# Kernel optimization log

Measured on AMD Instinct MI355X. Metric: run time of the kernel, lower is better.

The kernel has to match this reference:

```python
import jax, jax.numpy as jnp
import numpy as np
import math

N_HEADS = 16
EMBED = 1024
D_HEAD = EMBED // N_HEADS
B, L = 2, 2048


def setup_inputs() -> dict:
    key = jax.random.key(0)
    k1, k2, k3, k4, k5 = jax.random.split(key, 5)
    s = 0.02
    return {
        "x": jax.random.normal(k1, (B, L, EMBED), dtype=jnp.float32),
        "w_qkv": jax.random.normal(k2, (3 * EMBED, EMBED), dtype=jnp.float32) * s,
        "b_qkv": jax.random.normal(k3, (3 * EMBED,), dtype=jnp.float32) * s,
        "w_out": jax.random.normal(k4, (EMBED, EMBED), dtype=jnp.float32) * s,
        "b_out": jax.random.normal(k5, (EMBED,), dtype=jnp.float32) * s,
        "mask": 1,
    }


def reference(x, w_qkv, b_qkv, w_out, b_out, mask):
    b, l, e = x.shape
    qkv = x @ w_qkv.T + b_qkv                      # (B, L, 3E)
    q, k, v = jnp.split(qkv, 3, axis=-1)
    # (B, L, H, d) -> (B, H, L, d)
    q = q.reshape(b, l, N_HEADS, D_HEAD).transpose(0, 2, 1, 3)
    k = k.reshape(b, l, N_HEADS, D_HEAD).transpose(0, 2, 1, 3)
    v = v.reshape(b, l, N_HEADS, D_HEAD).transpose(0, 2, 1, 3)
    # NOTE: faithful to source bug -- scores use V, not K
    scores = jnp.einsum("bhld,bhmd->bhlm", q, v) * (1.0 / math.sqrt(D_HEAD))
    if mask:
        causal = jnp.triu(jnp.ones((l, l), dtype=bool), k=1)  # (L, L)
        scores = jnp.where(causal, -jnp.inf, scores)
    attn = jax.nn.softmax(scores, axis=-1)          # (B, H, L, L)
    out = jnp.einsum("bhlm,bhmd->bhld", attn, v)    # (B, H, L, d)
    # NOTE: faithful to source bug -- transpose(1,2) result discarded,
    # so reshape straight from (B, H, L, d) to (B, L, E)
    out = out.reshape(b, l, e)
    return out @ w_out.T + b_out
```

## Files before the change

kernel.cpp:

```cpp
#include <hip/hip_runtime.h>
#include <math.h>

constexpr int Lc = 2048, Ec = 1024, Hc = 16, Dc = 64;

typedef __attribute__((ext_vector_type(8))) short bf16x8;
typedef __attribute__((ext_vector_type(4))) float f32x4;
typedef unsigned short u16;
typedef unsigned int u32;

#define MFMA16(a, b, c) __builtin_amdgcn_mfma_f32_16x16x32_bf16(a, b, c, 0, 0, 0)

__device__ inline u16 f2bf(float f) {
  u32 u = __builtin_bit_cast(u32, f);
  u32 r = u + 0x7fff + ((u >> 16) & 1);
  return (u16)(r >> 16);
}

__device__ inline void gld16(const void* g, void* l) {
  __builtin_amdgcn_global_load_lds(
      (const __attribute__((address_space(1))) u32*)g,
      (__attribute__((address_space(3))) u32*)l, 16, 0, 0);
}

constexpr size_t XN = (size_t)4096 * 1024;
constexpr size_t WQN = (size_t)2048 * 1024;
constexpr size_t WON = (size_t)1024 * 1024;

__global__ __launch_bounds__(256) void convert_all(
    const float* __restrict__ x, const float* __restrict__ wqkv,
    const float* __restrict__ wout, u16* __restrict__ xb,
    u16* __restrict__ wqb, u16* __restrict__ wob)
{
  const size_t i = ((size_t)blockIdx.x * 256 + threadIdx.x) * 4;
  float4 v;
  u16* dst;
  if (i < XN) {
    v = *(const float4*)(x + i);
    dst = xb + i;
  } else if (i < XN + WQN) {
    const size_t off = i - XN;
    const size_t row = off >> 10, col = off & 1023;
    const size_t srow = row + ((row >> 10) << 10);
    v = *(const float4*)(wqkv + srow * 1024 + col);
    dst = wqb + off;
  } else {
    const size_t off = i - XN - WQN;
    v = *(const float4*)(wout + off);
    dst = wob + off;
  }
  u16 o0 = f2bf(v.x), o1 = f2bf(v.y), o2 = f2bf(v.z), o3 = f2bf(v.w);
  dst[0] = o0; dst[1] = o1; dst[2] = o2; dst[3] = o3;
}

__global__ __launch_bounds__(256) void gemm_qv(
    const u16* __restrict__ A, const u16* __restrict__ W,
    const float* __restrict__ bqkv, u16* __restrict__ Q, u16* __restrict__ V)
{
  __shared__ u16 As[128 * 32];
  __shared__ u16 Bs[128 * 32];
  const int tid = threadIdx.x;
  const int w = tid >> 6, lane = tid & 63;
  const int quad = lane >> 4, l16 = lane & 15;
  const int wm = w >> 1, wn = w & 1;
  const int rowTile = blockIdx.y * 128;
  const int colTile = blockIdx.x * 128;

  const int r0 = tid >> 2, o0 = (tid & 3) * 8;
  const u16* Ab0 = A + (size_t)(rowTile + r0) * 1024 + o0;
  const u16* Ab1 = A + (size_t)(rowTile + r0 + 64) * 1024 + o0;
  const u16* Bb0 = W + (size_t)(colTile + r0) * 1024 + o0;
  const u16* Bb1 = W + (size_t)(colTile + r0 + 64) * 1024 + o0;
  u16* lA0 = &As[(size_t)tid * 8];
  u16* lA1 = &As[(size_t)(tid + 256) * 8];
  u16* lB0 = &Bs[(size_t)tid * 8];
  u16* lB1 = &Bs[(size_t)(tid + 256) * 8];

  f32x4 acc[4][4] = {};

  for (int k0 = 0; k0 < 1024; k0 += 32) {
    __syncthreads();
    gld16(Ab0 + k0, lA0);
    gld16(Ab1 + k0, lA1);
    gld16(Bb0 + k0, lB0);
    gld16(Bb1 + k0, lB1);
    __syncthreads();
    bf16x8 af[4], bf[4];
#pragma unroll
    for (int s = 0; s < 4; ++s)
      af[s] = *(const bf16x8*)&As[(wm * 64 + s * 16 + l16) * 32 + quad * 8];
#pragma unroll
    for (int n = 0; n < 4; ++n)
      bf[n] = *(const bf16x8*)&Bs[(wn * 64 + n * 16 + l16) * 32 + quad * 8];
#pragma unroll
    for (int s = 0; s < 4; ++s)
#pragma unroll
      for (int n = 0; n < 4; ++n)
        acc[s][n] = MFMA16(af[s], bf[n], acc[s][n]);
  }

#pragma unroll
  for (int n = 0; n < 4; ++n) {
    const int gn = colTile + wn * 64 + n * 16 + l16;
    const bool isV = gn >= 1024;
    const float bias = bqkv[gn + (isV ? 1024 : 0)];
    const float scl = isV ? 1.0f : 0.125f;
    const int h = (gn & 1023) >> 6, d = gn & 63;
    u16* dst = isV ? V : Q;
#pragma unroll
    for (int s = 0; s < 4; ++s) {
#pragma unroll
      for (int r = 0; r < 4; ++r) {
        const int gm = rowTile + wm * 64 + s * 16 + quad * 4 + r;
        const int b = gm >> 11, l = gm & 2047;
        dst[(((size_t)(b * Hc + h)) * Lc + l) * Dc + d] = f2bf((acc[s][n][r] + bias) * scl);
      }
    }
  }
}

constexpr int VSTR = 72;
constexpr int VTSTR = 66;
constexpr int PSTR = 72;

__global__ __launch_bounds__(256) void attn_mfma(
    const u16* __restrict__ Q, const u16* __restrict__ V,
    u16* __restrict__ outA)
{
  __shared__ u16 Vs[64 * VSTR];
  __shared__ u16 VsT[64 * VTSTR];
  __shared__ u16 Ps[4][16 * PSTR];
  const int tid = threadIdx.x;
  const int w = tid >> 6, lane = tid & 63;
  const int quad = lane >> 4, l16 = lane & 15;
  const int bh = blockIdx.y;
  const int b = bh >> 4, h = bh & 15;
  const u16* Qb = Q + (size_t)bh * Lc * Dc;
  const u16* Vb = V + (size_t)bh * Lc * Dc;
  const int vr0 = tid >> 3, vd0 = (tid & 7) * 8;

  for (int half = 0; half < 2; ++half) {
    const int qt = half ? (31 - blockIdx.x) : blockIdx.x;
    const int q0 = qt * 64;
    const int nt = qt + 1;
    const int wqmin = q0 + w * 16;

    bf16x8 qf[2];
#pragma unroll
    for (int kk = 0; kk < 2; ++kk)
      qf[kk] = *(const bf16x8*)(Qb + (size_t)(q0 + w * 16 + l16) * 64 + kk * 32 + quad * 8);

    f32x4 O[4] = {};
    float lsum[4] = {0.f, 0.f, 0.f, 0.f};

    bf16x8 v0 = *(const bf16x8*)(Vb + (size_t)vr0 * 64 + vd0);
    bf16x8 v1 = *(const bf16x8*)(Vb + (size_t)(vr0 + 32) * 64 + vd0);

    for (int t = 0; t < nt; ++t) {
      const int kt = t * 64;
      __syncthreads();
      *(bf16x8*)&Vs[vr0 * VSTR + vd0] = v0;
      *(bf16x8*)&Vs[(vr0 + 32) * VSTR + vd0] = v1;
#pragma unroll
      for (int j = 0; j < 8; ++j) {
        VsT[(vd0 + j) * VTSTR + vr0] = (u16)v0[j];
        VsT[(vd0 + j) * VTSTR + vr0 + 32] = (u16)v1[j];
      }
      if (t + 1 < nt) {
        v0 = *(const bf16x8*)(Vb + (size_t)(kt + 64 + vr0) * 64 + vd0);
        v1 = *(const bf16x8*)(Vb + (size_t)(kt + 96 + vr0) * 64 + vd0);
      }
      __syncthreads();
      if (kt > wqmin + 15) continue;

      f32x4 sf[4] = {};
      bf16x8 bvf[2][4];
#pragma unroll
      for (int nb = 0; nb < 4; ++nb)
#pragma unroll
        for (int kk = 0; kk < 2; ++kk)
          bvf[kk][nb] = *(const bf16x8*)&Vs[(nb * 16 + l16) * VSTR + kk * 32 + quad * 8];
#pragma unroll
      for (int nb = 0; nb < 4; ++nb) {
        sf[nb] = MFMA16(qf[0], bvf[0][nb], sf[nb]);
        sf[nb] = MFMA16(qf[1], bvf[1][nb], sf[nb]);
      }

      const bool needmask = (kt + 63 > wqmin);
#pragma unroll
      for (int nb = 0; nb < 4; ++nb)
#pragma unroll
        for (int r = 0; r < 4; ++r) {
          float p = __expf(sf[nb][r]);
          if (needmask) {
            const int key = kt + nb * 16 + l16;
            const int qr = wqmin + quad * 4 + r;
            if (key > qr) p = 0.f;
          }
          lsum[r] += p;
          Ps[w][(quad * 4 + r) * PSTR + nb * 16 + l16] = f2bf(p);
        }

      bf16x8 pf[2];
#pragma unroll
      for (int kk = 0; kk < 2; ++kk)
        pf[kk] = *(const bf16x8*)&Ps[w][l16 * PSTR + kk * 32 + quad * 8];
#pragma unroll
      for (int db = 0; db < 4; ++db) {
        O[db] = MFMA16(pf[0], *(const bf16x8*)&VsT[(db * 16 + l16) * VTSTR + quad * 8], O[db]);
        O[db] = MFMA16(pf[1], *(const bf16x8*)&VsT[(db * 16 + l16) * VTSTR + 32 + quad * 8], O[db]);
      }
    }

#pragma unroll
    for (int r = 0; r < 4; ++r) {
      float l = lsum[r];
      l += __shfl_xor(l, 1);
      l += __shfl_xor(l, 2);
      l += __shfl_xor(l, 4);
      l += __shfl_xor(l, 8);
      const float inv = 1.f / l;
      const int q = q0 + w * 16 + quad * 4 + r;
      const int orow = h * 128 + (q >> 4);
      const int cbase = (q & 15) << 6;
#pragma unroll
      for (int db = 0; db < 4; ++db)
        outA[((size_t)b * Lc + orow) * Ec + cbase + db * 16 + l16] =
            f2bf(O[db][r] * inv);
    }
  }
}

__global__ __launch_bounds__(256) void gemm_out(
    const u16* __restrict__ A, const u16* __restrict__ W,
    const float* __restrict__ bias, float* __restrict__ out)
{
  __shared__ u16 As[128 * 32];
  __shared__ u16 Bs[128 * 32];
  const int tid = threadIdx.x;
  const int w = tid >> 6, lane = tid & 63;
  const int quad = lane >> 4, l16 = lane & 15;
  const int wm = w >> 1, wn = w & 1;
  const int rowTile = blockIdx.y * 128;
  const int colTile = blockIdx.x * 128;

  const int r0 = tid >> 2, o0 = (tid & 3) * 8;
  const u16* Ab0 = A + (size_t)(rowTile + r0) * 1024 + o0;
  const u16* Ab1 = A + (size_t)(rowTile + r0 + 64) * 1024 + o0;
  const u16* Bb0 = W + (size_t)(colTile + r0) * 1024 + o0;
  const u16* Bb1 = W + (size_t)(colTile + r0 + 64) * 1024 + o0;
  u16* lA0 = &As[(size_t)tid * 8];
  u16* lA1 = &As[(size_t)(tid + 256) * 8];
  u16* lB0 = &Bs[(size_t)tid * 8];
  u16* lB1 = &Bs[(size_t)(tid + 256) * 8];

  f32x4 acc[4][4] = {};

  for (int k0 = 0; k0 < 1024; k0 += 32) {
    __syncthreads();
    gld16(Ab0 + k0, lA0);
    gld16(Ab1 + k0, lA1);
    gld16(Bb0 + k0, lB0);
    gld16(Bb1 + k0, lB1);
    __syncthreads();
    bf16x8 af[4], bf[4];
#pragma unroll
    for (int s = 0; s < 4; ++s)
      af[s] = *(const bf16x8*)&As[(wm * 64 + s * 16 + l16) * 32 + quad * 8];
#pragma unroll
    for (int n = 0; n < 4; ++n)
      bf[n] = *(const bf16x8*)&Bs[(wn * 64 + n * 16 + l16) * 32 + quad * 8];
#pragma unroll
    for (int s = 0; s < 4; ++s)
#pragma unroll
      for (int n = 0; n < 4; ++n)
        acc[s][n] = MFMA16(af[s], bf[n], acc[s][n]);
  }

#pragma unroll
  for (int n = 0; n < 4; ++n) {
    const int gn = colTile + wn * 64 + n * 16 + l16;
    const float bn = bias[gn];
#pragma unroll
    for (int s = 0; s < 4; ++s)
#pragma unroll
      for (int r = 0; r < 4; ++r) {
        const int gm = rowTile + wm * 64 + s * 16 + quad * 4 + r;
        out[(size_t)gm * 1024 + gn] = acc[s][n][r] + bn;
      }
  }
}

extern "C" void kernel_launch(void* const* d_in, const int* in_sizes, int n_in,
                              void* d_out, int out_size, void* d_ws, size_t ws_size,
                              hipStream_t stream) {
  (void)in_sizes; (void)n_in; (void)out_size; (void)ws_size;
  const float* x     = (const float*)d_in[0];
  const float* w_qkv = (const float*)d_in[1];
  const float* b_qkv = (const float*)d_in[2];
  const float* w_out = (const float*)d_in[3];
  const float* b_out = (const float*)d_in[4];
  float* out = (float*)d_out;

  u16* xb  = (u16*)d_ws;
  u16* wqb = xb + XN;
  u16* wob = wqb + WQN;
  u16* Qw  = wob + WON;
  u16* Vw  = Qw + (size_t)2 * Hc * Lc * Dc;
  u16* Aw  = Vw + (size_t)2 * Hc * Lc * Dc;

  convert_all<<<7168, 256, 0, stream>>>(x, w_qkv, w_out, xb, wqb, wob);
  gemm_qv<<<dim3(16, 32), 256, 0, stream>>>(xb, wqb, b_qkv, Qw, Vw);
  attn_mfma<<<dim3(16, 32), 256, 0, stream>>>(Qw, Vw, Aw);
  gemm_out<<<dim3(8, 32), 256, 0, stream>>>(Aw, wob, b_out, out);
}
```

Baseline: 193.4 us.

## Restructure attention to 256-query blocks with transposed MFMA and smaller out-GEMM tiles

The attention kernel now gives each block 256 queries and each wave 64 rows. It computes S^T with V fragments taken straight from global memory, stages only a swizzled transposed V tile in LDS, and writes P with packed stores. This drops the untransposed V staging and the two-half load-balancing loop, and reuses each V tile across four query subtiles. It also removes the LDS bank conflicts on VsT. Because blocks now cover causal ranges of very different length, the load may be less balanced. The output GEMM tile shrinks to 64x128 so more blocks are launched.

```diff
diff --git a/kernel.cpp b/kernel.cpp
--- a/kernel.cpp
+++ b/kernel.cpp
@@ -118,114 +118,130 @@
   }
 }
 
-constexpr int VSTR = 72;
-constexpr int VTSTR = 66;
-constexpr int PSTR = 72;
-
-__global__ __launch_bounds__(256) void attn_mfma(
+constexpr int VTSTR = 72;
+constexpr int PSTR = 88;
+
+__global__ __launch_bounds__(256, 1) void attn_mfma(
     const u16* __restrict__ Q, const u16* __restrict__ V,
     u16* __restrict__ outA)
 {
-  __shared__ u16 Vs[64 * VSTR];
   __shared__ u16 VsT[64 * VTSTR];
-  __shared__ u16 Ps[4][16 * PSTR];
+  __shared__ u16 Ps[256 * PSTR];
   const int tid = threadIdx.x;
   const int w = tid >> 6, lane = tid & 63;
   const int quad = lane >> 4, l16 = lane & 15;
+  const int q0 = blockIdx.x * 256;
   const int bh = blockIdx.y;
   const int b = bh >> 4, h = bh & 15;
   const u16* Qb = Q + (size_t)bh * Lc * Dc;
   const u16* Vb = V + (size_t)bh * Lc * Dc;
+  const int wq0 = q0 + w * 64;
+  const int nt = (q0 >> 6) + 4;
+
+  bf16x8 qf[4][2];
+#pragma unroll
+  for (int s = 0; s < 4; ++s)
+#pragma unroll
+    for (int kk = 0; kk < 2; ++kk)
+      qf[s][kk] = *(const bf16x8*)(Qb + (size_t)(wq0 + s * 16 + l16) * 64 + kk * 32 + quad * 8);
+
+  f32x4 O[4][4] = {};
+  float lsum[4] = {0.f, 0.f, 0.f, 0.f};
+
   const int vr0 = tid >> 3, vd0 = (tid & 7) * 8;
-
-  for (int half = 0; half < 2; ++half) {
-    const int qt = half ? (31 - blockIdx.x) : blockIdx.x;
-    const int q0 = qt * 64;
-    const int nt = qt + 1;
-    const int wqmin = q0 + w * 16;
-
-    bf16x8 qf[2];
+  bf16x8 v0 = *(const bf16x8*)(Vb + (size_t)vr0 * 64 + vd0);
+  bf16x8 v1 = *(const bf16x8*)(Vb + (size_t)(vr0 + 32) * 64 + vd0);
+  bf16x8 av[4][2];
+#pragma unroll
+  for (int nb = 0; nb < 4; ++nb)
 #pragma unroll
     for (int kk = 0; kk < 2; ++kk)
-      qf[kk] = *(const bf16x8*)(Qb + (size_t)(q0 + w * 16 + l16) * 64 + kk * 32 + quad * 8);
-
-    f32x4 O[4] = {};
-    float lsum[4] = {0.f, 0.f, 0.f, 0.f};
-
-    bf16x8 v0 = *(const bf16x8*)(Vb + (size_t)vr0 * 64 + vd0);
-    bf16x8 v1 = *(const bf16x8*)(Vb + (size_t)(vr0 + 32) * 64 + vd0);
-
-    for (int t = 0; t < nt; ++t) {
-      const int kt = t * 64;
-      __syncthreads();
-      *(bf16x8*)&Vs[vr0 * VSTR + vd0] = v0;
-      *(bf16x8*)&Vs[(vr0 + 32) * VSTR + vd0] = v1;
-#pragma unroll
-      for (int j = 0; j < 8; ++j) {
-        VsT[(vd0 + j) * VTSTR + vr0] = (u16)v0[j];
-        VsT[(vd0 + j) * VTSTR + vr0 + 32] = (u16)v1[j];
-      }
-      if (t + 1 < nt) {
-        v0 = *(const bf16x8*)(Vb + (size_t)(kt + 64 + vr0) * 64 + vd0);
-        v1 = *(const bf16x8*)(Vb + (size_t)(kt + 96 + vr0) * 64 + vd0);
-      }
-      __syncthreads();
-      if (kt > wqmin + 15) continue;
-
+      av[nb][kk] = *(const bf16x8*)(Vb + (size_t)(nb * 16 + l16) * 64 + kk * 32 + quad * 8);
+
+  for (int t = 0; t < nt; ++t) {
+    const int kt = t * 64;
+    __syncthreads();
+#pragma unroll
+    for (int j = 0; j < 8; ++j) {
+      const int d = vd0 + j, sw = d & 0x38;
+      VsT[d * VTSTR + (vr0 ^ sw)] = (u16)v0[j];
+      VsT[d * VTSTR + ((vr0 + 32) ^ sw)] = (u16)v1[j];
+    }
+    if (t + 1 < nt) {
+      v0 = *(const bf16x8*)(Vb + (size_t)(kt + 64 + vr0) * 64 + vd0);
+      v1 = *(const bf16x8*)(Vb + (size_t)(kt + 96 + vr0) * 64 + vd0);
+    }
+    __syncthreads();
+    if (kt > wq0) continue;
+
+    const bool diag = (kt == wq0);
+#pragma unroll
+    for (int s = 0; s < 4; ++s) {
       f32x4 sf[4] = {};
-      bf16x8 bvf[2][4];
+#pragma unroll
+      for (int nb = 0; nb < 4; ++nb) {
+        sf[nb] = MFMA16(av[nb][0], qf[s][0], sf[nb]);
+        sf[nb] = MFMA16(av[nb][1], qf[s][1], sf[nb]);
+      }
+#pragma unroll
+      for (int nb = 0; nb < 4; ++nb) {
+        float p[4];
+#pragma unroll
+        for (int r = 0; r < 4; ++r) {
+          float pv = __expf(sf[nb][r]);
+          if (diag && (nb * 16 + quad * 4 + r > s * 16 + l16)) pv = 0.f;
+          p[r] = pv;
+          lsum[s] += pv;
+        }
+        const u32 lo = (u32)f2bf(p[0]) | ((u32)f2bf(p[1]) << 16);
+        const u32 hi = (u32)f2bf(p[2]) | ((u32)f2bf(p[3]) << 16);
+        *(uint2*)&Ps[(size_t)(w * 64 + s * 16 + l16) * PSTR + nb * 16 + quad * 4] =
+            make_uint2(lo, hi);
+      }
+    }
+    if (kt + 64 <= wq0) {
 #pragma unroll
       for (int nb = 0; nb < 4; ++nb)
 #pragma unroll
         for (int kk = 0; kk < 2; ++kk)
-          bvf[kk][nb] = *(const bf16x8*)&Vs[(nb * 16 + l16) * VSTR + kk * 32 + quad * 8];
-#pragma unroll
-      for (int nb = 0; nb < 4; ++nb) {
-        sf[nb] = MFMA16(qf[0], bvf[0][nb], sf[nb]);
-        sf[nb] = MFMA16(qf[1], bvf[1][nb], sf[nb]);
-      }
-
-      const bool needmask = (kt + 63 > wqmin);
-#pragma unroll
-      for (int nb = 0; nb < 4; ++nb)
-#pragma unroll
-        for (int r = 0; r < 4; ++r) {
-          float p = __expf(sf[nb][r]);
-          if (needmask) {
-            const int key = kt + nb * 16 + l16;
-            const int qr = wqmin + quad * 4 + r;
-            if (key > qr) p = 0.f;
-          }
-          lsum[r] += p;
-          Ps[w][(quad * 4 + r) * PSTR + nb * 16 + l16] = f2bf(p);
-        }
-
-      bf16x8 pf[2];
-#pragma unroll
-      for (int kk = 0; kk < 2; ++kk)
-        pf[kk] = *(const bf16x8*)&Ps[w][l16 * PSTR + kk * 32 + quad * 8];
-#pragma unroll
-      for (int db = 0; db < 4; ++db) {
-        O[db] = MFMA16(pf[0], *(const bf16x8*)&VsT[(db * 16 + l16) * VTSTR + quad * 8], O[db]);
-        O[db] = MFMA16(pf[1], *(const bf16x8*)&VsT[(db * 16 + l16) * VTSTR + 32 + quad * 8], O[db]);
-      }
-    }
-
-#pragma unroll
-    for (int r = 0; r < 4; ++r) {
-      float l = lsum[r];
-      l += __shfl_xor(l, 1);
-      l += __shfl_xor(l, 2);
-      l += __shfl_xor(l, 4);
-      l += __shfl_xor(l, 8);
-      const float inv = 1.f / l;
-      const int q = q0 + w * 16 + quad * 4 + r;
-      const int orow = h * 128 + (q >> 4);
-      const int cbase = (q & 15) << 6;
-#pragma unroll
-      for (int db = 0; db < 4; ++db)
-        outA[((size_t)b * Lc + orow) * Ec + cbase + db * 16 + l16] =
-            f2bf(O[db][r] * inv);
+          av[nb][kk] = *(const bf16x8*)(Vb + (size_t)(kt + 64 + nb * 16 + l16) * 64 + kk * 32 + quad * 8);
+    }
+    __asm__ volatile("s_waitcnt lgkmcnt(0)");
+
+    bf16x8 vt[4][2], pb[4][2];
+#pragma unroll
+    for (int db = 0; db < 4; ++db) {
+      const int d = db * 16 + l16, sw = d & 0x38;
+      vt[db][0] = *(const bf16x8*)&VsT[d * VTSTR + ((quad * 8) ^ sw)];
+      vt[db][1] = *(const bf16x8*)&VsT[d * VTSTR + ((32 + quad * 8) ^ sw)];
+    }
+#pragma unroll
+    for (int s = 0; s < 4; ++s) {
+      pb[s][0] = *(const bf16x8*)&Ps[(size_t)(w * 64 + s * 16 + l16) * PSTR + quad * 8];
+      pb[s][1] = *(const bf16x8*)&Ps[(size_t)(w * 64 + s * 16 + l16) * PSTR + 32 + quad * 8];
+    }
+#pragma unroll
+    for (int db = 0; db < 4; ++db)
+#pragma unroll
+      for (int s = 0; s < 4; ++s) {
+        O[db][s] = MFMA16(vt[db][0], pb[s][0], O[db][s]);
+        O[db][s] = MFMA16(vt[db][1], pb[s][1], O[db][s]);
+      }
+  }
+
+#pragma unroll
+  for (int s = 0; s < 4; ++s) {
+    float l = lsum[s];
+    l += __shfl_xor(l, 16);
+    l += __shfl_xor(l, 32);
+    const float inv = 1.f / l;
+    const int row = h * 128 + (wq0 >> 4) + s;
+    const size_t base = ((size_t)b * Lc + row) * Ec;
+#pragma unroll
+    for (int db = 0; db < 4; ++db) {
+      const u32 lo = (u32)f2bf(O[db][s][0] * inv) | ((u32)f2bf(O[db][s][1] * inv) << 16);
+      const u32 hi = (u32)f2bf(O[db][s][2] * inv) | ((u32)f2bf(O[db][s][3] * inv) << 16);
+      *(uint2*)(outA + base + l16 * 64 + db * 16 + quad * 4) = make_uint2(lo, hi);
     }
   }
 }
@@ -234,43 +250,40 @@
     const u16* __restrict__ A, const u16* __restrict__ W,
     const float* __restrict__ bias, float* __restrict__ out)
 {
-  __shared__ u16 As[128 * 32];
+  __shared__ u16 As[64 * 32];
   __shared__ u16 Bs[128 * 32];
   const int tid = threadIdx.x;
   const int w = tid >> 6, lane = tid & 63;
   const int quad = lane >> 4, l16 = lane & 15;
-  const int wm = w >> 1, wn = w & 1;
-  const int rowTile = blockIdx.y * 128;
+  const int wm = w & 1, wn = w >> 1;
+  const int rowTile = blockIdx.y * 64;
   const int colTile = blockIdx.x * 128;
 
   const int r0 = tid >> 2, o0 = (tid & 3) * 8;
   const u16* Ab0 = A + (size_t)(rowTile + r0) * 1024 + o0;
-  const u16* Ab1 = A + (size_t)(rowTile + r0 + 64) * 1024 + o0;
   const u16* Bb0 = W + (size_t)(colTile + r0) * 1024 + o0;
   const u16* Bb1 = W + (size_t)(colTile + r0 + 64) * 1024 + o0;
   u16* lA0 = &As[(size_t)tid * 8];
-  u16* lA1 = &As[(size_t)(tid + 256) * 8];
   u16* lB0 = &Bs[(size_t)tid * 8];
   u16* lB1 = &Bs[(size_t)(tid + 256) * 8];
 
-  f32x4 acc[4][4] = {};
+  f32x4 acc[2][4] = {};
 
   for (int k0 = 0; k0 < 1024; k0 += 32) {
     __syncthreads();
     gld16(Ab0 + k0, lA0);
-    gld16(Ab1 + k0, lA1);
     gld16(Bb0 + k0, lB0);
     gld16(Bb1 + k0, lB1);
     __syncthreads();
-    bf16x8 af[4], bf[4];
-#pragma unroll
-    for (int s = 0; s < 4; ++s)
-      af[s] = *(const bf16x8*)&As[(wm * 64 + s * 16 + l16) * 32 + quad * 8];
+    bf16x8 af[2], bf[4];
+#pragma unroll
+    for (int s = 0; s < 2; ++s)
+      af[s] = *(const bf16x8*)&As[(wm * 32 + s * 16 + l16) * 32 + quad * 8];
 #pragma unroll
     for (int n = 0; n < 4; ++n)
       bf[n] = *(const bf16x8*)&Bs[(wn * 64 + n * 16 + l16) * 32 + quad * 8];
 #pragma unroll
-    for (int s = 0; s < 4; ++s)
+    for (int s = 0; s < 2; ++s)
 #pragma unroll
       for (int n = 0; n < 4; ++n)
         acc[s][n] = MFMA16(af[s], bf[n], acc[s][n]);
@@ -281,10 +294,10 @@
     const int gn = colTile + wn * 64 + n * 16 + l16;
     const float bn = bias[gn];
 #pragma unroll
-    for (int s = 0; s < 4; ++s)
+    for (int s = 0; s < 2; ++s)
 #pragma unroll
       for (int r = 0; r < 4; ++r) {
-        const int gm = rowTile + wm * 64 + s * 16 + quad * 4 + r;
+        const int gm = rowTile + wm * 32 + s * 16 + quad * 4 + r;
         out[(size_t)gm * 1024 + gn] = acc[s][n][r] + bn;
       }
   }
@@ -310,6 +323,6 @@
 
   convert_all<<<7168, 256, 0, stream>>>(x, w_qkv, w_out, xb, wqb, wob);
   gemm_qv<<<dim3(16, 32), 256, 0, stream>>>(xb, wqb, b_qkv, Qw, Vw);
-  attn_mfma<<<dim3(16, 32), 256, 0, stream>>>(Qw, Vw, Aw);
-  gemm_out<<<dim3(8, 32), 256, 0, stream>>>(Aw, wob, b_out, out);
-}
+  attn_mfma<<<dim3(8, 32), 256, 0, stream>>>(Qw, Vw, Aw);
+  gemm_out<<<dim3(8, 64), 256, 0, stream>>>(Aw, wob, b_out, out);
+}
```

Result: slower. 209.8 us (+8.5%).
